# Kernel tuning notes

Hardware: AMD Instinct MI355X
Metric: run time of the kernel (lower is better)

## Reference

```python
import jax, jax.numpy as jnp
import numpy as np

N_NODES = 100000
N_EDGES = 6400000


def setup_inputs() -> dict:
    key = jax.random.key(0)
    k1, k2, k3, k4, k5, k6 = jax.random.split(key, 6)
    x = jax.random.normal(k1, (N_NODES, 10), dtype=jnp.float32)
    edge_index = jax.random.randint(k2, (2, N_EDGES), 0, N_NODES, dtype=jnp.int64)
    # GCNConv(10,16) and GCNConv(16,2) parameters (glorot-ish scale)
    W1 = jax.random.normal(k3, (10, 16), dtype=jnp.float32) * (1.0 / np.sqrt(10))
    b1 = jnp.zeros((16,), dtype=jnp.float32)
    W2 = jax.random.normal(k4, (16, 2), dtype=jnp.float32) * (1.0 / np.sqrt(16))
    b2 = jnp.zeros((2,), dtype=jnp.float32)
    return {"x": x, "edge_index": edge_index, "W1": W1, "b1": b1, "W2": W2, "b2": b2}


def _gcn_conv(h, src, dst, norm, W, b, n_nodes):
    # PyG GCNConv: linear first, then normalized scatter-add aggregation
    h = h @ W                                   # [N, out]
    msg = h[src] * norm[:, None]                # gather + per-edge scale
    out = jax.ops.segment_sum(msg, dst, num_segments=n_nodes)
    return out + b


def reference(x, edge_index, W1, b1, W2, b2):
    n_nodes = x.shape[0]
    loop = jnp.arange(n_nodes, dtype=edge_index.dtype)
    src = jnp.concatenate([edge_index[0], loop])  # self-loops added (PyG default)
    dst = jnp.concatenate([edge_index[1], loop])
    # symmetric normalization deg^{-1/2} A_hat deg^{-1/2} (deg from target index)
    deg = jax.ops.segment_sum(jnp.ones_like(dst, dtype=x.dtype), dst, num_segments=n_nodes)
    dinv = jnp.where(deg > 0, jax.lax.rsqrt(deg), 0.0)
    norm = dinv[src] * dinv[dst]                 # [E+N]
    h = _gcn_conv(x, src, dst, norm, W1, b1, n_nodes)
    h = jax.nn.relu(h)
    out = _gcn_conv(h, src, dst, norm, W2, b2, n_nodes)
    return out
```

## Files before the change

kernel.cpp:

```cpp
#include <hip/hip_runtime.h>


#define BKT_BITS  8
#define BKT_SZ    256
#define NBK       512
#define NBLKA     256
#define TPB_A     1024
#define DST_SHIFT 24
#define SRC_MASK  0xFFFFFFu
#define XS_STRIDE 16

static __device__ __forceinline__ int get_src(const void* ei, int is64, int n_edges, unsigned e) {
    return is64 ? (int)((const long long*)ei)[e] : ((const int*)ei)[e];
}
static __device__ __forceinline__ int get_dst(const void* ei, int is64, int n_edges, unsigned e) {
    return is64 ? (int)((const long long*)ei)[(unsigned)n_edges + e]
                : ((const int*)ei)[(unsigned)n_edges + e];
}

static __global__ void detect64_kernel(const unsigned int* __restrict__ w, int* flag) {
    __shared__ int nz;
    if (threadIdx.x == 0) nz = 0;
    __syncthreads();
    int local = 0;
    for (int k = threadIdx.x; k < 4096; k += blockDim.x)
        if (w[2 * k + 1] != 0u) local = 1;
    if (local) atomicOr(&nz, 1);
    __syncthreads();
    if (threadIdx.x == 0) *flag = (nz == 0) ? 1 : 0;
}

static __global__ void histA_kernel(const void* __restrict__ ei, const int* __restrict__ flag,
                                    unsigned* __restrict__ histA, int n_edges) {
    __shared__ unsigned h[NBK];
    for (int i = threadIdx.x; i < NBK; i += TPB_A) h[i] = 0u;
    __syncthreads();
    const int is64 = *flag;
    unsigned stride = gridDim.x * blockDim.x;
    for (unsigned e = blockIdx.x * blockDim.x + threadIdx.x; e < (unsigned)n_edges; e += stride) {
        int d = get_dst(ei, is64, n_edges, e);
        atomicAdd(&h[(unsigned)d >> BKT_BITS], 1u);
    }
    __syncthreads();
    for (int i = threadIdx.x; i < NBK; i += TPB_A)
        histA[blockIdx.x * NBK + i] = h[i];
}

static __global__ void scan1_kernel(unsigned* __restrict__ histA, unsigned* __restrict__ total) {
    __shared__ unsigned s0[NBLKA], s1[NBLKA];
    const int b = blockIdx.x;
    const int t = threadIdx.x;
    unsigned v = histA[t * NBK + b];
    unsigned* a = s0; unsigned* c = s1;
    a[t] = v;
    __syncthreads();
    for (int off = 1; off < NBLKA; off <<= 1) {
        c[t] = a[t] + (t >= off ? a[t - off] : 0u);
        __syncthreads();
        unsigned* tmp = a; a = c; c = tmp;
    }
    histA[t * NBK + b] = a[t] - v;
    if (t == NBLKA - 1) total[b] = a[NBLKA - 1];
}

static __global__ void scan2_kernel(const unsigned* __restrict__ total,
                                    unsigned* __restrict__ bucket_base) {
    __shared__ unsigned s0[NBK], s1[NBK];
    const int t = threadIdx.x;
    unsigned v = total[t];
    unsigned* a = s0; unsigned* c = s1;
    a[t] = v;
    __syncthreads();
    for (int off = 1; off < NBK; off <<= 1) {
        c[t] = a[t] + (t >= off ? a[t - off] : 0u);
        __syncthreads();
        unsigned* tmp = a; a = c; c = tmp;
    }
    bucket_base[t] = a[t] - v;
}

static __global__ void scatterA_kernel(const void* __restrict__ ei, const int* __restrict__ flag,
                                       const unsigned* __restrict__ histA,
                                       const unsigned* __restrict__ bucket_base,
                                       unsigned* __restrict__ bucketed, int n_edges) {
    __shared__ unsigned cur[NBK];
    for (int i = threadIdx.x; i < NBK; i += TPB_A)
        cur[i] = bucket_base[i] + histA[blockIdx.x * NBK + i];
    __syncthreads();
    const int is64 = *flag;
    unsigned stride = gridDim.x * blockDim.x;
    for (unsigned e = blockIdx.x * blockDim.x + threadIdx.x; e < (unsigned)n_edges; e += stride) {
        unsigned s = (unsigned)get_src(ei, is64, n_edges, e);
        unsigned d = (unsigned)get_dst(ei, is64, n_edges, e);
        unsigned pos = atomicAdd(&cur[d >> BKT_BITS], 1u);
        bucketed[pos] = s | ((d & (BKT_SZ - 1u)) << DST_SHIFT);
    }
}

static __global__ void passB_kernel(const unsigned* __restrict__ bucketed,
                                    const unsigned* __restrict__ total,
                                    const unsigned* __restrict__ bucket_base,
                                    const float* __restrict__ x,
                                    unsigned* __restrict__ csr_src,
                                    unsigned* __restrict__ row_start,
                                    unsigned* __restrict__ cnt,
                                    float* __restrict__ dinv,
                                    float* __restrict__ xs, int n_nodes) {
    const int b = blockIdx.x;
    const int n0 = b << BKT_BITS;
    const int t = threadIdx.x;
    const unsigned base = bucket_base[b];
    const unsigned count = total[b];

    __shared__ unsigned h[BKT_SZ];
    __shared__ unsigned s0[BKT_SZ], s1[BKT_SZ];
    __shared__ unsigned cur[BKT_SZ];
    h[t] = 0u;
    __syncthreads();
    for (unsigned k = t; k < count; k += BKT_SZ)
        atomicAdd(&h[bucketed[base + k] >> DST_SHIFT], 1u);
    __syncthreads();
    unsigned* a = s0; unsigned* c = s1;
    a[t] = h[t];
    __syncthreads();
    for (int off = 1; off < BKT_SZ; off <<= 1) {
        c[t] = a[t] + (t >= off ? a[t - off] : 0u);
        __syncthreads();
        unsigned* tmp = a; a = c; c = tmp;
    }
    unsigned excl = a[t] - h[t];
    cur[t] = excl;
    int n = n0 + t;
    if (n < n_nodes) {
        row_start[n] = base + excl;
        cnt[n] = h[t];
        float di = rsqrtf((float)(h[t] + 1u));
        dinv[n] = di;
        float v[10];
#pragma unroll
        for (int j = 0; j < 10; j++) v[j] = x[(size_t)n * 10 + j] * di;
        float4* xr = (float4*)(xs + (size_t)n * XS_STRIDE);
        xr[0] = make_float4(v[0], v[1], v[2], v[3]);
        xr[1] = make_float4(v[4], v[5], v[6], v[7]);
        xr[2] = make_float4(v[8], v[9], 0.f, 0.f);
        xr[3] = make_float4(0.f, 0.f, 0.f, 0.f);
    }
    __syncthreads();
    for (unsigned k = t; k < count; k += BKT_SZ) {
        unsigned w = bucketed[base + k];
        unsigned pos = base + atomicAdd(&cur[w >> DST_SHIFT], 1u);
        csr_src[pos] = w & SRC_MASK;
    }
}

static __global__ void node1_kernel(const float* __restrict__ x, const float* __restrict__ dinv,
                                    float* __restrict__ xs, int n_nodes) {
    int i = blockIdx.x * blockDim.x + threadIdx.x;
    if (i >= n_nodes) return;
    float di = dinv[i];
    float v[10];
#pragma unroll
    for (int j = 0; j < 10; j++) v[j] = x[(size_t)i * 10 + j] * di;
    float4* xr = (float4*)(xs + (size_t)i * XS_STRIDE);
    xr[0] = make_float4(v[0], v[1], v[2], v[3]);
    xr[1] = make_float4(v[4], v[5], v[6], v[7]);
    xr[2] = make_float4(v[8], v[9], 0.f, 0.f);
    xr[3] = make_float4(0.f, 0.f, 0.f, 0.f);
}

static __global__ void gather1_kernel(const unsigned int* __restrict__ row_start,
                                      const unsigned int* __restrict__ cnt,
                                      const unsigned int* __restrict__ csr_src,
                                      const float* __restrict__ xs,
                                      const float* __restrict__ dinv,
                                      const float* __restrict__ W1, const float* __restrict__ b1,
                                      const float* __restrict__ W2,
                                      float* __restrict__ gs, int n_nodes) {
    __shared__ float sW1[160];
    __shared__ float sb1[16];
    __shared__ float sW2[32];
    for (int k = threadIdx.x; k < 160; k += blockDim.x) sW1[k] = W1[k];
    if (threadIdx.x < 16) sb1[threadIdx.x] = b1[threadIdx.x];
    if (threadIdx.x < 32) sW2[threadIdx.x] = W2[threadIdx.x];
    __syncthreads();
    int node = blockIdx.x * (blockDim.x >> 4) + (threadIdx.x >> 4);
    int lg = threadIdx.x & 15;
    if (node >= n_nodes) return;
    unsigned start = row_start[node];
    unsigned degn = cnt[node];
    float acc[10];
#pragma unroll
    for (int j = 0; j < 10; j++) acc[j] = 0.f;
    const float4* X = (const float4*)xs;
    for (unsigned k = lg; k < degn; k += 16) {
        unsigned s = csr_src[start + k];
        float4 v0 = X[s * 4 + 0];
        float4 v1 = X[s * 4 + 1];
        float4 v2 = X[s * 4 + 2];
        acc[0] += v0.x; acc[1] += v0.y; acc[2] += v0.z; acc[3] += v0.w;
        acc[4] += v1.x; acc[5] += v1.y; acc[6] += v1.z; acc[7] += v1.w;
        acc[8] += v2.x; acc[9] += v2.y;
    }
    if (lg == 0) {
        float4 v0 = X[(size_t)node * 4 + 0];
        float4 v1 = X[(size_t)node * 4 + 1];
        float4 v2 = X[(size_t)node * 4 + 2];
        acc[0] += v0.x; acc[1] += v0.y; acc[2] += v0.z; acc[3] += v0.w;
        acc[4] += v1.x; acc[5] += v1.y; acc[6] += v1.z; acc[7] += v1.w;
        acc[8] += v2.x; acc[9] += v2.y;
    }
#pragma unroll
    for (int off = 8; off > 0; off >>= 1) {
#pragma unroll
        for (int j = 0; j < 10; j++) acc[j] += __shfl_xor(acc[j], off);
    }
    float di = dinv[node];
    float h = sb1[lg];
#pragma unroll
    for (int k = 0; k < 10; k++) h = fmaf(acc[k] * di, sW1[k * 16 + lg], h);
    h = fmaxf(h, 0.f);
    float g0 = h * sW2[lg * 2 + 0];
    float g1 = h * sW2[lg * 2 + 1];
#pragma unroll
    for (int off = 8; off > 0; off >>= 1) {
        g0 += __shfl_xor(g0, off);
        g1 += __shfl_xor(g1, off);
    }
    if (lg == 0) {
        float2 o;
        o.x = g0 * di;
        o.y = g1 * di;
        ((float2*)gs)[node] = o;
    }
}

static __global__ void gather2_kernel(const unsigned int* __restrict__ row_start,
                                      const unsigned int* __restrict__ cnt,
                                      const unsigned int* __restrict__ csr_src,
                                      const float* __restrict__ gs,
                                      const float* __restrict__ dinv,
                                      const float* __restrict__ b2,
                                      float* __restrict__ out, int n_nodes) {
    int node = blockIdx.x * (blockDim.x >> 4) + (threadIdx.x >> 4);
    int lg = threadIdx.x & 15;
    if (node >= n_nodes) return;
    unsigned start = row_start[node];
    unsigned degn = cnt[node];
    float a0 = 0.f, a1 = 0.f;
    const float2* G = (const float2*)gs;
    for (unsigned k = lg; k < degn; k += 16) {
        float2 v = G[csr_src[start + k]];
        a0 += v.x; a1 += v.y;
    }
    if (lg == 0) {
        float2 s = G[node];
        a0 += s.x; a1 += s.y;
    }
#pragma unroll
    for (int off = 8; off > 0; off >>= 1) {
        a0 += __shfl_xor(a0, off);
        a1 += __shfl_xor(a1, off);
    }
    if (lg == 0) {
        float di = dinv[node];
        float2 o;
        o.x = fmaf(a0, di, b2[0]);
        o.y = fmaf(a1, di, b2[1]);
        ((float2*)out)[node] = o;
    }
}

static __global__ void deg_kernel(const void* __restrict__ ei, const int* __restrict__ flag,
                                  unsigned int* __restrict__ cnt, int n_edges) {
    const int is64 = *flag;
    unsigned stride = gridDim.x * blockDim.x;
    for (unsigned e = blockIdx.x * blockDim.x + threadIdx.x; e < (unsigned)n_edges; e += stride) {
        int d = get_dst(ei, is64, n_edges, e);
        atomicAdd(&cnt[d], 1u);
    }
}
static __global__ void alloc_kernel(const unsigned int* __restrict__ cnt,
                                    unsigned int* __restrict__ row_start,
                                    unsigned int* __restrict__ cursor,
                                    unsigned int* __restrict__ gcur,
                                    float* __restrict__ dinv, int n_nodes) {
    __shared__ unsigned wsum[4];
    int i = blockIdx.x * blockDim.x + threadIdx.x;
    int lane = threadIdx.x & 63;
    int wid = threadIdx.x >> 6;
    unsigned d = (i < n_nodes) ? cnt[i] : 0u;
    unsigned scan = d;
#pragma unroll
    for (int off = 1; off < 64; off <<= 1) {
        unsigned t = __shfl_up(scan, off);
        if (lane >= off) scan += t;
    }
    if (lane == 63) wsum[wid] = scan;
    __syncthreads();
    if (threadIdx.x == 0) {
        unsigned s0 = wsum[0], s1 = wsum[1], s2 = wsum[2], s3 = wsum[3];
        unsigned base = atomicAdd(gcur, s0 + s1 + s2 + s3);
        wsum[0] = base;
        wsum[1] = base + s0;
        wsum[2] = base + s0 + s1;
        wsum[3] = base + s0 + s1 + s2;
    }
    __syncthreads();
    if (i < n_nodes) {
        unsigned pos = wsum[wid] + scan - d;
        row_start[i] = pos;
        cursor[i] = pos;
        dinv[i] = rsqrtf((float)(d + 1u));
    }
}
static __global__ void csrfill_kernel(const void* __restrict__ ei, const int* __restrict__ flag,
                                      unsigned int* __restrict__ cursor,
                                      unsigned int* __restrict__ csr_src, int n_edges) {
    const int is64 = *flag;
    unsigned stride = gridDim.x * blockDim.x;
    for (unsigned e = blockIdx.x * blockDim.x + threadIdx.x; e < (unsigned)n_edges; e += stride) {
        int s = get_src(ei, is64, n_edges, e);
        int d = get_dst(ei, is64, n_edges, e);
        unsigned pos = atomicAdd(&cursor[d], 1u);
        csr_src[pos] = (unsigned)s;
    }
}

static inline char* align_up(char* p, size_t a) {
    return (char*)(((uintptr_t)p + a - 1) & ~(uintptr_t)(a - 1));
}

extern "C" void kernel_launch(void* const* d_in, const int* in_sizes, int n_in,
                              void* d_out, int out_size, void* d_ws, size_t ws_size,
                              hipStream_t stream) {
    const float* x  = (const float*)d_in[0];
    const void*  ei = d_in[1];
    const float* W1 = (const float*)d_in[2];
    const float* b1 = (const float*)d_in[3];
    const float* W2 = (const float*)d_in[4];
    const float* b2 = (const float*)d_in[5];
    float* out = (float*)d_out;

    const int n_nodes = in_sizes[0] / 10;
    const int n_edges = in_sizes[1] / 2;
    (void)n_in; (void)out_size;

    const int nbuckets = (n_nodes + BKT_SZ - 1) >> BKT_BITS;
    const bool pack_ok = (n_nodes <= (1 << DST_SHIFT)) && (nbuckets <= NBK);

    char* p = (char*)d_ws;
    int* flag = (int*)p;
    unsigned* gcur = (unsigned*)(p + 64);
    p += 256;
    unsigned* row_start = (unsigned*)p; p = align_up(p + (size_t)n_nodes * 4, 256);
    unsigned* cnt = (unsigned*)p;       p = align_up(p + (size_t)n_nodes * 4, 256);
    float* dinv = (float*)p;            p = align_up(p + (size_t)n_nodes * 4, 256);
    float* gs = (float*)p;              p = align_up(p + (size_t)n_nodes * 8, 256);
    float* xs = (float*)p;              p = align_up(p + (size_t)n_nodes * 4 * XS_STRIDE, 256);
    unsigned* csr_src = (unsigned*)p;   p = align_up(p + (size_t)n_edges * 4, 256);

    const size_t base_bytes = (size_t)(p - (char*)d_ws);
    const size_t need_new = base_bytes + (size_t)NBLKA * NBK * 4 + 2 * (size_t)NBK * 4 + 1024 +
                            (size_t)n_edges * 4;
    const size_t need_old = base_bytes + (size_t)n_nodes * 4 + 256;

    const int NODES_PER_BLK = 256 / 16;
    const int gblocks = (n_nodes + NODES_PER_BLK - 1) / NODES_PER_BLK;

    if (pack_ok && ws_size >= need_new) {
        unsigned* histA = (unsigned*)p;       p = align_up(p + (size_t)NBLKA * NBK * 4, 256);
        unsigned* total = (unsigned*)p;       p = align_up(p + (size_t)NBK * 4, 256);
        unsigned* bucket_base = (unsigned*)p; p = align_up(p + (size_t)NBK * 4, 256);
        unsigned* bucketed = (unsigned*)p;    p = align_up(p + (size_t)n_edges * 4, 256);

        detect64_kernel<<<1, 256, 0, stream>>>((const unsigned int*)ei, flag);
        histA_kernel<<<NBLKA, TPB_A, 0, stream>>>(ei, flag, histA, n_edges);
        scan1_kernel<<<NBK, NBLKA, 0, stream>>>(histA, total);
        scan2_kernel<<<1, NBK, 0, stream>>>(total, bucket_base);
        scatterA_kernel<<<NBLKA, TPB_A, 0, stream>>>(ei, flag, histA, bucket_base, bucketed, n_edges);
        passB_kernel<<<nbuckets, BKT_SZ, 0, stream>>>(bucketed, total, bucket_base, x, csr_src,
                                                      row_start, cnt, dinv, xs, n_nodes);
        gather1_kernel<<<gblocks, 256, 0, stream>>>(row_start, cnt, csr_src, xs, dinv,
                                                    W1, b1, W2, gs, n_nodes);
        gather2_kernel<<<gblocks, 256, 0, stream>>>(row_start, cnt, csr_src, gs, dinv,
                                                    b2, out, n_nodes);
    } else if (ws_size >= need_old) {
        unsigned* cursor = (unsigned*)p;

        hipMemsetAsync(d_ws, 0, 256, stream);
        hipMemsetAsync(cnt, 0, (size_t)n_nodes * 4, stream);
        detect64_kernel<<<1, 256, 0, stream>>>((const unsigned int*)ei, flag);
        deg_kernel<<<2048, 256, 0, stream>>>(ei, flag, cnt, n_edges);
        alloc_kernel<<<(n_nodes + 255) / 256, 256, 0, stream>>>(cnt, row_start, cursor, gcur, dinv, n_nodes);
        csrfill_kernel<<<4096, 256, 0, stream>>>(ei, flag, cursor, csr_src, n_edges);
        node1_kernel<<<(n_nodes + 255) / 256, 256, 0, stream>>>(x, dinv, xs, n_nodes);
        gather1_kernel<<<gblocks, 256, 0, stream>>>(row_start, cnt, csr_src, xs, dinv,
                                                    W1, b1, W2, gs, n_nodes);
        gather2_kernel<<<gblocks, 256, 0, stream>>>(row_start, cnt, csr_src, gs, dinv,
                                                    b2, out, n_nodes);
    }
}
```

Before: 216.5 us.

## Store scaled features as fp16, use nontemporal loads, widen passB blocks

Normalized node features are packed as half-precision pairs into 32-byte rows instead of 64-byte fp32 rows, halving the bytes gathered per edge in the first aggregation. Edge-index and CSR reads now use nontemporal loads so streaming data does not displace the cached feature table. passB runs with 512 threads per bucket so its histogram and scatter loops have more parallelism. The fp16 storage lowers accuracy of the layer-1 inputs and may move results against the reference tolerance.

New measurement: 243.2 us. +12.3%, slower.

```diff
diff --git a/kernel.cpp b/kernel.cpp
--- a/kernel.cpp
+++ b/kernel.cpp
@@ -1,4 +1,5 @@
 #include <hip/hip_runtime.h>
+#include <hip/hip_fp16.h>
 
 
 #define BKT_BITS  8
@@ -6,16 +7,23 @@
 #define NBK       512
 #define NBLKA     256
 #define TPB_A     1024
+#define TPB_B     512
 #define DST_SHIFT 24
 #define SRC_MASK  0xFFFFFFu
-#define XS_STRIDE 16
-
-static __device__ __forceinline__ int get_src(const void* ei, int is64, int n_edges, unsigned e) {
-    return is64 ? (int)((const long long*)ei)[e] : ((const int*)ei)[e];
-}
-static __device__ __forceinline__ int get_dst(const void* ei, int is64, int n_edges, unsigned e) {
-    return is64 ? (int)((const long long*)ei)[(unsigned)n_edges + e]
-                : ((const int*)ei)[(unsigned)n_edges + e];
+#define XS_BYTES  32
+
+static __device__ __forceinline__ int nt_src(const void* ei, int is64, int n_edges, unsigned e) {
+    return is64 ? (int)__builtin_nontemporal_load(&((const long long*)ei)[e])
+                : __builtin_nontemporal_load(&((const int*)ei)[e]);
+}
+static __device__ __forceinline__ int nt_dst(const void* ei, int is64, int n_edges, unsigned e) {
+    return is64 ? (int)__builtin_nontemporal_load(&((const long long*)ei)[(unsigned)n_edges + e])
+                : __builtin_nontemporal_load(&((const int*)ei)[(unsigned)n_edges + e]);
+}
+
+static __device__ __forceinline__ float2 h2f(unsigned w) {
+    __half2 h = *(__half2*)&w;
+    return __half22float2(h);
 }
 
 static __global__ void detect64_kernel(const unsigned int* __restrict__ w, int* flag) {
@@ -38,7 +46,7 @@
     const int is64 = *flag;
     unsigned stride = gridDim.x * blockDim.x;
     for (unsigned e = blockIdx.x * blockDim.x + threadIdx.x; e < (unsigned)n_edges; e += stride) {
-        int d = get_dst(ei, is64, n_edges, e);
+        int d = nt_dst(ei, is64, n_edges, e);
         atomicAdd(&h[(unsigned)d >> BKT_BITS], 1u);
     }
     __syncthreads();
@@ -90,8 +98,8 @@
     const int is64 = *flag;
     unsigned stride = gridDim.x * blockDim.x;
     for (unsigned e = blockIdx.x * blockDim.x + threadIdx.x; e < (unsigned)n_edges; e += stride) {
-        unsigned s = (unsigned)get_src(ei, is64, n_edges, e);
-        unsigned d = (unsigned)get_dst(ei, is64, n_edges, e);
+        unsigned s = (unsigned)nt_src(ei, is64, n_edges, e);
+        unsigned d = (unsigned)nt_dst(ei, is64, n_edges, e);
         unsigned pos = atomicAdd(&cur[d >> BKT_BITS], 1u);
         bucketed[pos] = s | ((d & (BKT_SZ - 1u)) << DST_SHIFT);
     }
@@ -105,7 +113,7 @@
                                     unsigned* __restrict__ row_start,
                                     unsigned* __restrict__ cnt,
                                     float* __restrict__ dinv,
-                                    float* __restrict__ xs, int n_nodes) {
+                                    char* __restrict__ xs, int n_nodes) {
     const int b = blockIdx.x;
     const int n0 = b << BKT_BITS;
     const int t = threadIdx.x;
@@ -115,38 +123,42 @@
     __shared__ unsigned h[BKT_SZ];
     __shared__ unsigned s0[BKT_SZ], s1[BKT_SZ];
     __shared__ unsigned cur[BKT_SZ];
-    h[t] = 0u;
-    __syncthreads();
-    for (unsigned k = t; k < count; k += BKT_SZ)
+    if (t < BKT_SZ) h[t] = 0u;
+    __syncthreads();
+    for (unsigned k = t; k < count; k += TPB_B)
         atomicAdd(&h[bucketed[base + k] >> DST_SHIFT], 1u);
     __syncthreads();
     unsigned* a = s0; unsigned* c = s1;
-    a[t] = h[t];
+    if (t < BKT_SZ) a[t] = h[t];
     __syncthreads();
     for (int off = 1; off < BKT_SZ; off <<= 1) {
-        c[t] = a[t] + (t >= off ? a[t - off] : 0u);
+        if (t < BKT_SZ) c[t] = a[t] + (t >= off ? a[t - off] : 0u);
         __syncthreads();
         unsigned* tmp = a; a = c; c = tmp;
     }
-    unsigned excl = a[t] - h[t];
-    cur[t] = excl;
-    int n = n0 + t;
-    if (n < n_nodes) {
-        row_start[n] = base + excl;
-        cnt[n] = h[t];
-        float di = rsqrtf((float)(h[t] + 1u));
-        dinv[n] = di;
-        float v[10];
-#pragma unroll
-        for (int j = 0; j < 10; j++) v[j] = x[(size_t)n * 10 + j] * di;
-        float4* xr = (float4*)(xs + (size_t)n * XS_STRIDE);
-        xr[0] = make_float4(v[0], v[1], v[2], v[3]);
-        xr[1] = make_float4(v[4], v[5], v[6], v[7]);
-        xr[2] = make_float4(v[8], v[9], 0.f, 0.f);
-        xr[3] = make_float4(0.f, 0.f, 0.f, 0.f);
-    }
-    __syncthreads();
-    for (unsigned k = t; k < count; k += BKT_SZ) {
+    if (t < BKT_SZ) {
+        unsigned excl = a[t] - h[t];
+        cur[t] = excl;
+        int n = n0 + t;
+        if (n < n_nodes) {
+            row_start[n] = base + excl;
+            cnt[n] = h[t];
+            float di = rsqrtf((float)(h[t] + 1u));
+            dinv[n] = di;
+            unsigned w[5];
+#pragma unroll
+            for (int j = 0; j < 5; j++) {
+                unsigned lo = __half_as_ushort(__float2half_rn(x[(size_t)n * 10 + 2 * j] * di));
+                unsigned hi = __half_as_ushort(__float2half_rn(x[(size_t)n * 10 + 2 * j + 1] * di));
+                w[j] = lo | (hi << 16);
+            }
+            char* row = xs + (size_t)n * XS_BYTES;
+            *(uint4*)row = make_uint4(w[0], w[1], w[2], w[3]);
+            *(uint2*)(row + 16) = make_uint2(w[4], 0u);
+        }
+    }
+    __syncthreads();
+    for (unsigned k = t; k < count; k += TPB_B) {
         unsigned w = bucketed[base + k];
         unsigned pos = base + atomicAdd(&cur[w >> DST_SHIFT], 1u);
         csr_src[pos] = w & SRC_MASK;
@@ -154,24 +166,26 @@
 }
 
 static __global__ void node1_kernel(const float* __restrict__ x, const float* __restrict__ dinv,
-                                    float* __restrict__ xs, int n_nodes) {
+                                    char* __restrict__ xs, int n_nodes) {
     int i = blockIdx.x * blockDim.x + threadIdx.x;
     if (i >= n_nodes) return;
     float di = dinv[i];
-    float v[10];
-#pragma unroll
-    for (int j = 0; j < 10; j++) v[j] = x[(size_t)i * 10 + j] * di;
-    float4* xr = (float4*)(xs + (size_t)i * XS_STRIDE);
-    xr[0] = make_float4(v[0], v[1], v[2], v[3]);
-    xr[1] = make_float4(v[4], v[5], v[6], v[7]);
-    xr[2] = make_float4(v[8], v[9], 0.f, 0.f);
-    xr[3] = make_float4(0.f, 0.f, 0.f, 0.f);
+    unsigned w[5];
+#pragma unroll
+    for (int j = 0; j < 5; j++) {
+        unsigned lo = __half_as_ushort(__float2half_rn(x[(size_t)i * 10 + 2 * j] * di));
+        unsigned hi = __half_as_ushort(__float2half_rn(x[(size_t)i * 10 + 2 * j + 1] * di));
+        w[j] = lo | (hi << 16);
+    }
+    char* row = xs + (size_t)i * XS_BYTES;
+    *(uint4*)row = make_uint4(w[0], w[1], w[2], w[3]);
+    *(uint2*)(row + 16) = make_uint2(w[4], 0u);
 }
 
 static __global__ void gather1_kernel(const unsigned int* __restrict__ row_start,
                                       const unsigned int* __restrict__ cnt,
                                       const unsigned int* __restrict__ csr_src,
-                                      const float* __restrict__ xs,
+                                      const char* __restrict__ xs,
                                       const float* __restrict__ dinv,
                                       const float* __restrict__ W1, const float* __restrict__ b1,
                                       const float* __restrict__ W2,
@@ -191,23 +205,28 @@
     float acc[10];
 #pragma unroll
     for (int j = 0; j < 10; j++) acc[j] = 0.f;
-    const float4* X = (const float4*)xs;
     for (unsigned k = lg; k < degn; k += 16) {
-        unsigned s = csr_src[start + k];
-        float4 v0 = X[s * 4 + 0];
-        float4 v1 = X[s * 4 + 1];
-        float4 v2 = X[s * 4 + 2];
-        acc[0] += v0.x; acc[1] += v0.y; acc[2] += v0.z; acc[3] += v0.w;
-        acc[4] += v1.x; acc[5] += v1.y; acc[6] += v1.z; acc[7] += v1.w;
-        acc[8] += v2.x; acc[9] += v2.y;
+        unsigned s = __builtin_nontemporal_load(&csr_src[start + k]);
+        const char* row = xs + (size_t)s * XS_BYTES;
+        uint4 a = *(const uint4*)row;
+        unsigned b = *(const unsigned*)(row + 16);
+        float2 f;
+        f = h2f(a.x); acc[0] += f.x; acc[1] += f.y;
+        f = h2f(a.y); acc[2] += f.x; acc[3] += f.y;
+        f = h2f(a.z); acc[4] += f.x; acc[5] += f.y;
+        f = h2f(a.w); acc[6] += f.x; acc[7] += f.y;
+        f = h2f(b);   acc[8] += f.x; acc[9] += f.y;
     }
     if (lg == 0) {
-        float4 v0 = X[(size_t)node * 4 + 0];
-        float4 v1 = X[(size_t)node * 4 + 1];
-        float4 v2 = X[(size_t)node * 4 + 2];
-        acc[0] += v0.x; acc[1] += v0.y; acc[2] += v0.z; acc[3] += v0.w;
-        acc[4] += v1.x; acc[5] += v1.y; acc[6] += v1.z; acc[7] += v1.w;
-        acc[8] += v2.x; acc[9] += v2.y;
+        const char* row = xs + (size_t)node * XS_BYTES;
+        uint4 a = *(const uint4*)row;
+        unsigned b = *(const unsigned*)(row + 16);
+        float2 f;
+        f = h2f(a.x); acc[0] += f.x; acc[1] += f.y;
+        f = h2f(a.y); acc[2] += f.x; acc[3] += f.y;
+        f = h2f(a.z); acc[4] += f.x; acc[5] += f.y;
+        f = h2f(a.w); acc[6] += f.x; acc[7] += f.y;
+        f = h2f(b);   acc[8] += f.x; acc[9] += f.y;
     }
 #pragma unroll
     for (int off = 8; off > 0; off >>= 1) {
@@ -249,7 +268,8 @@
     float a0 = 0.f, a1 = 0.f;
     const float2* G = (const float2*)gs;
     for (unsigned k = lg; k < degn; k += 16) {
-        float2 v = G[csr_src[start + k]];
+        unsigned s = __builtin_nontemporal_load(&csr_src[start + k]);
+        float2 v = G[s];
         a0 += v.x; a1 += v.y;
     }
     if (lg == 0) {
@@ -275,7 +295,7 @@
     const int is64 = *flag;
     unsigned stride = gridDim.x * blockDim.x;
     for (unsigned e = blockIdx.x * blockDim.x + threadIdx.x; e < (unsigned)n_edges; e += stride) {
-        int d = get_dst(ei, is64, n_edges, e);
+        int d = nt_dst(ei, is64, n_edges, e);
         atomicAdd(&cnt[d], 1u);
     }
 }
@@ -319,8 +339,8 @@
     const int is64 = *flag;
     unsigned stride = gridDim.x * blockDim.x;
     for (unsigned e = blockIdx.x * blockDim.x + threadIdx.x; e < (unsigned)n_edges; e += stride) {
-        int s = get_src(ei, is64, n_edges, e);
-        int d = get_dst(ei, is64, n_edges, e);
+        int s = nt_src(ei, is64, n_edges, e);
+        int d = nt_dst(ei, is64, n_edges, e);
         unsigned pos = atomicAdd(&cursor[d], 1u);
         csr_src[pos] = (unsigned)s;
     }
@@ -356,7 +376,7 @@
     unsigned* cnt = (unsigned*)p;       p = align_up(p + (size_t)n_nodes * 4, 256);
     float* dinv = (float*)p;            p = align_up(p + (size_t)n_nodes * 4, 256);
     float* gs = (float*)p;              p = align_up(p + (size_t)n_nodes * 8, 256);
-    float* xs = (float*)p;              p = align_up(p + (size_t)n_nodes * 4 * XS_STRIDE, 256);
+    char* xs = p;                       p = align_up(p + (size_t)n_nodes * XS_BYTES, 256);
     unsigned* csr_src = (unsigned*)p;   p = align_up(p + (size_t)n_edges * 4, 256);
 
     const size_t base_bytes = (size_t)(p - (char*)d_ws);
@@ -378,8 +398,8 @@
         scan1_kernel<<<NBK, NBLKA, 0, stream>>>(histA, total);
         scan2_kernel<<<1, NBK, 0, stream>>>(total, bucket_base);
         scatterA_kernel<<<NBLKA, TPB_A, 0, stream>>>(ei, flag, histA, bucket_base, bucketed, n_edges);
-        passB_kernel<<<nbuckets, BKT_SZ, 0, stream>>>(bucketed, total, bucket_base, x, csr_src,
-                                                      row_start, cnt, dinv, xs, n_nodes);
+        passB_kernel<<<nbuckets, TPB_B, 0, stream>>>(bucketed, total, bucket_base, x, csr_src,
+                                                     row_start, cnt, dinv, xs, n_nodes);
         gather1_kernel<<<gblocks, 256, 0, stream>>>(row_start, cnt, csr_src, xs, dinv,
                                                     W1, b1, W2, gs, n_nodes);
         gather2_kernel<<<gblocks, 256, 0, stream>>>(row_start, cnt, csr_src, gs, dinv,
```
